# Optimization experiments

Measured on AMD Instinct MI355X. Metric: run time of the kernel, lower is better.

The kernel has to match this reference:

```python
import jax, jax.numpy as jnp
import numpy as np

B, S, D, I, E = 2, 2048, 1024, 2048, 8
AUX_COEF, Z_COEF = 0.01, 0.001


def setup_inputs() -> dict:
    key = jax.random.key(0)
    ks = jax.random.split(key, 5)
    sd = np.float32(1.0 / np.sqrt(D))
    si = np.float32(1.0 / np.sqrt(I))
    return {
        "hidden_states": jax.random.normal(ks[0], (B, S, D), jnp.float32),
        "gate_w": jax.random.normal(ks[1], (D, E), jnp.float32) * sd,
        "w_gate": jax.random.normal(ks[2], (E, D, I), jnp.float32) * sd,
        "w_up": jax.random.normal(ks[3], (E, D, I), jnp.float32) * sd,
        "w_down": jax.random.normal(ks[4], (E, I, D), jnp.float32) * si,
        "pressure_bias": jnp.zeros((E,), jnp.float32),
        "temperature_field": jnp.ones((E,), jnp.float32),
    }


def reference(hidden_states, gate_w, w_gate, w_up, w_down, pressure_bias, temperature_field):
    b, s, d = hidden_states.shape
    e = gate_w.shape[1]
    x = hidden_states.reshape(-1, d)  # [T, D]

    # Router with P/T geometry: logits' = (logits + P) / clamp(T)
    logits = x @ gate_w + pressure_bias
    temp = jnp.clip(temperature_field, 0.1, 10.0)
    logits = logits / temp
    probs = jax.nn.softmax(logits, axis=-1)  # [T, E]
    routing_weights = jnp.max(probs, axis=-1)  # [T]
    selected = jnp.argmax(probs, axis=-1)      # [T] int

    # Load balancing + z-loss
    onehot = jax.nn.one_hot(selected, e, dtype=probs.dtype)
    f_i = onehot.mean(axis=0)          # fraction of tokens per expert
    P_i = probs.mean(axis=0)           # mean routing prob per expert
    load_balance = e * jnp.sum(f_i * P_i)
    z_loss = jnp.mean(jax.nn.logsumexp(logits, axis=-1) ** 2)
    aux_loss = AUX_COEF * load_balance + Z_COEF * z_loss

    # Top-1 dispatch/combine: row-wise SwiGLU FFN, mask non-selected rows.
    out = jnp.zeros_like(x)
    for ei in range(e):  # small fixed expert count
        y = (jax.nn.silu(x @ w_gate[ei]) * (x @ w_up[ei])) @ w_down[ei]
        out = out + jnp.where((selected == ei)[:, None], y * routing_weights[:, None], 0.0)

    return out.reshape(b, s, d), aux_loss
```

## Files before the change

kernel.cpp:

```cpp
#include <hip/hip_runtime.h>
#include <stdint.h>
#include <stddef.h>

#define T_TOK 4096
#define D_DIM 1024
#define I_DIM 2048
#define E_EXP 8

#define MAXT64  (T_TOK / 64 + E_EXP)
#define MAXT128 (T_TOK / 128 + E_EXP)
#define CAP (T_TOK + E_EXP * 128)

#define BT 64
#define NK1 (D_DIM / BT)
#define NC1 (I_DIM / BT)
#define G1_BLOCKS (MAXT64 * NC1)
#define BM2 128
#define BN2 64
#define BK2 64
#define NK2 (I_DIM / BK2)
#define NC2 (D_DIM / BN2)

typedef __attribute__((ext_vector_type(4))) float f32x4;
typedef __attribute__((ext_vector_type(4))) short s16x4;
typedef __attribute__((ext_vector_type(8))) short s16x8;
typedef __attribute__((ext_vector_type(2))) unsigned int u32x2;

__device__ __forceinline__ unsigned short f2bf(float f) {
    union { float f; unsigned u; } v; v.f = f;
    unsigned u = v.u;
    return (unsigned short)((u + 0x7fffu + ((u >> 16) & 1u)) >> 16);
}

__device__ __forceinline__ void gll16(const void* g, void* l) {
    __builtin_amdgcn_global_load_lds(
        (const __attribute__((address_space(1))) void*)g,
        (__attribute__((address_space(3))) void*)l, 16, 0, 0);
}

__global__ void k_init(int* idxl, int* counts, int* fill, float* sumP, float* lse2) {
    int tid = blockIdx.x * blockDim.x + threadIdx.x;
    for (int i = tid; i < CAP; i += blockDim.x * gridDim.x) idxl[i] = -1;
    if (blockIdx.x == 0 && threadIdx.x < E_EXP) {
        counts[threadIdx.x] = 0;
        fill[threadIdx.x] = 0;
        sumP[threadIdx.x] = 0.f;
    }
    if (blockIdx.x == 0 && threadIdx.x == 0) lse2[0] = 0.f;
}

__device__ void router_block(
    const float* __restrict__ x, const float* __restrict__ gw,
    const float* __restrict__ pb, const float* __restrict__ tf,
    unsigned short* __restrict__ xb, int* __restrict__ selected,
    float* __restrict__ rw, int* __restrict__ counts,
    float* __restrict__ sumP, float* __restrict__ lse2)
{
    int gwave = (blockIdx.x * 256 + threadIdx.x) >> 6;
    int lane = threadIdx.x & 63;

    float aP[E_EXP];
    int aC[E_EXP];
    float aZ = 0.f;
#pragma unroll
    for (int e = 0; e < E_EXP; e++) { aP[e] = 0.f; aC[e] = 0; }

    float tcl[E_EXP], pbv[E_EXP];
#pragma unroll
    for (int e = 0; e < E_EXP; e++) {
        tcl[e] = fminf(fmaxf(tf[e], 0.1f), 10.f);
        pbv[e] = pb[e];
    }

    for (int ti = 0; ti < 16; ++ti) {
        int t = gwave * 16 + ti;
        const float* xr = x + (size_t)t * D_DIM;
        float s[E_EXP];
#pragma unroll
        for (int e = 0; e < E_EXP; e++) s[e] = 0.f;

#pragma unroll
        for (int j = 0; j < 4; j++) {
            int d0 = j * 256 + lane * 4;
            f32x4 xv = *(const f32x4*)(xr + d0);
            s16x4 xs;
#pragma unroll
            for (int i = 0; i < 4; i++) xs[i] = (short)f2bf(xv[i]);
            *(s16x4*)(xb + (size_t)t * D_DIM + d0) = xs;
#pragma unroll
            for (int i = 0; i < 4; i++) {
                const float* gr = gw + (size_t)(d0 + i) * E_EXP;
                f32x4 g0 = *(const f32x4*)(gr);
                f32x4 g1 = *(const f32x4*)(gr + 4);
                float xi = xv[i];
                s[0] += xi * g0[0]; s[1] += xi * g0[1];
                s[2] += xi * g0[2]; s[3] += xi * g0[3];
                s[4] += xi * g1[0]; s[5] += xi * g1[1];
                s[6] += xi * g1[2]; s[7] += xi * g1[3];
            }
        }
#pragma unroll
        for (int m = 1; m < 64; m <<= 1) {
#pragma unroll
            for (int e = 0; e < E_EXP; e++) s[e] += __shfl_xor(s[e], m, 64);
        }
        float lg[E_EXP];
        float mx = -3.4e38f;
#pragma unroll
        for (int e = 0; e < E_EXP; e++) {
            lg[e] = (s[e] + pbv[e]) / tcl[e];
            mx = fmaxf(mx, lg[e]);
        }
        float p[E_EXP];
        float den = 0.f;
#pragma unroll
        for (int e = 0; e < E_EXP; e++) { p[e] = expf(lg[e] - mx); den += p[e]; }
        int sel = 0;
        float best = lg[0];
#pragma unroll
        for (int e = 1; e < E_EXP; e++) if (lg[e] > best) { best = lg[e]; sel = e; }
        float inv = 1.f / den;
        if (lane == 0) {
            selected[t] = sel;
            rw[t] = p[sel] * inv;
#pragma unroll
            for (int e = 0; e < E_EXP; e++) aP[e] += p[e] * inv;
            aC[sel] += 1;
            float lse = mx + logf(den);
            aZ += lse * lse;
        }
    }
    if (lane == 0) {
#pragma unroll
        for (int e = 0; e < E_EXP; e++) {
            atomicAdd(&sumP[e], aP[e]);
            if (aC[e]) atomicAdd(&counts[e], aC[e]);
        }
        atomicAdd(lse2, aZ);
    }
}

__device__ void conv_tile(const float* __restrict__ src, unsigned short* __restrict__ dst,
                          int R, int C, int rt, int ct, unsigned short* tb)
{
    int r0 = rt * 128, c0 = ct * 128;
    int tid = threadIdx.x;
    int rr = tid >> 5;
    int cc = (tid & 31) * 4;

#pragma unroll
    for (int p = 0; p < 16; ++p) {
        int r = p * 8 + rr;
        f32x4 v = *(const f32x4*)(src + (size_t)(r0 + r) * C + c0 + cc);
        s16x4 w;
#pragma unroll
        for (int i = 0; i < 4; ++i) w[i] = (short)f2bf(v[i]);
        *(s16x4*)(tb + r * 130 + cc) = w;
    }
    __syncthreads();

    int rb = (tid & 15) * 4;
    int cp = (tid >> 4) * 2;
#pragma unroll
    for (int p = 0; p < 8; ++p) {
        int rh = (p & 1) * 64;
        int c = (p >> 1) * 32 + cp;
        int rbase = rh + rb;
        unsigned int a0 = *(const unsigned int*)(tb + (rbase + 0) * 130 + c);
        unsigned int a1 = *(const unsigned int*)(tb + (rbase + 1) * 130 + c);
        unsigned int a2 = *(const unsigned int*)(tb + (rbase + 2) * 130 + c);
        unsigned int a3 = *(const unsigned int*)(tb + (rbase + 3) * 130 + c);
        u32x2 lo, hi;
        lo[0] = (a0 & 0xffffu) | (a1 << 16);
        lo[1] = (a2 & 0xffffu) | (a3 << 16);
        hi[0] = (a0 >> 16) | (a1 & 0xffff0000u);
        hi[1] = (a2 >> 16) | (a3 & 0xffff0000u);
        *(u32x2*)(dst + (size_t)(c0 + c) * R + r0 + rbase) = lo;
        *(u32x2*)(dst + (size_t)(c0 + c + 1) * R + r0 + rbase) = hi;
    }
}

__global__ __launch_bounds__(256) void k_fused1(
    const float* __restrict__ x, const float* __restrict__ gw,
    const float* __restrict__ pb, const float* __restrict__ tf,
    unsigned short* __restrict__ xb, int* __restrict__ selected,
    float* __restrict__ rw, int* __restrict__ counts,
    float* __restrict__ sumP, float* __restrict__ lse2,
    const float* __restrict__ wg, const float* __restrict__ wu,
    unsigned short* __restrict__ wgT, unsigned short* __restrict__ wuT)
{
    __shared__ unsigned short tb[128 * 130];
    int bid = blockIdx.x;
    if (bid < 64) {
        router_block(x, gw, pb, tf, xb, selected, rw, counts, sumP, lse2);
        return;
    }
    int b = bid - 64;
    if (b < 1024) {
        int e = b >> 7, t = b & 127;
        conv_tile(wg + (size_t)e * D_DIM * I_DIM, wgT + (size_t)e * D_DIM * I_DIM,
                  D_DIM, I_DIM, t >> 4, t & 15, tb);
    } else {
        b -= 1024;
        int e = b >> 7, t = b & 127;
        conv_tile(wu + (size_t)e * D_DIM * I_DIM, wuT + (size_t)e * D_DIM * I_DIM,
                  D_DIM, I_DIM, t >> 4, t & 15, tb);
    }
}

__global__ void k_setup(const int* counts, int* segst,
                        int* t128e, int* t128b, int* t64e, int* t64b) {
    if (threadIdx.x == 0 && blockIdx.x == 0) {
        int off = 0, a = 0, b = 0;
        for (int e = 0; e < E_EXP; e++) {
            segst[e] = off;
            int n = counts[e];
            int n128 = (n + 127) >> 7;
            int n64 = (n + 63) >> 6;
            for (int i = 0; i < n128; i++) { t128e[a] = e; t128b[a] = off + i * 128; a++; }
            for (int i = 0; i < n64; i++)  { t64e[b] = e;  t64b[b] = off + i * 64;  b++; }
            off += n128 * 128;
        }
        for (; a < MAXT128; ++a) { t128e[a] = -1; t128b[a] = 0; }
        for (; b < MAXT64; ++b)  { t64e[b] = -1;  t64b[b] = 0; }
    }
}

__global__ void k_scatter(const int* selected, const int* segst, int* fill, int* idxl) {
    int t = blockIdx.x * 256 + threadIdx.x;
    if (t < T_TOK) {
        int e = selected[t];
        int p = atomicAdd(&fill[e], 1);
        idxl[segst[e] + p] = t;
    }
}

__global__ __launch_bounds__(256) void k_fused2(
    const unsigned short* __restrict__ xb,
    const unsigned short* __restrict__ wgT,
    const int* __restrict__ idxl,
    const int* __restrict__ t64e, const int* __restrict__ t64b,
    unsigned short* __restrict__ H,
    const float* __restrict__ wd, unsigned short* __restrict__ wdT)
{
    __shared__ union {
        struct {
            unsigned short As[2][BT * BT];
            unsigned short Bg[2][BT * BT];
            unsigned short Bu[2][BT * BT];
        } g;
        unsigned short tb[128 * 130];
    } sm;

    int bid = blockIdx.x;
    int gid;
    if (bid < 2048) {
        if (bid & 1) {
            int b = bid >> 1;
            int e = b >> 7, t = b & 127;
            conv_tile(wd + (size_t)e * I_DIM * D_DIM, wdT + (size_t)e * I_DIM * D_DIM,
                      I_DIM, D_DIM, t >> 3, t & 7, sm.tb);
            return;
        }
        gid = bid >> 1;
    } else {
        gid = 1024 + (bid - 2048);
    }

    int rt = gid >> 5;
    int ct = gid & 31;
    int e = t64e[rt];
    if (e < 0) return;
    int base = t64b[rt];

    int tid = threadIdx.x;
    int l = tid & 63;
    int w = tid >> 6;
    int rsub = l >> 3;
    int csw = ((l & 7) ^ rsub) * 8;

    int tk0 = idxl[base + w * 16 + rsub];     tk0 = tk0 < 0 ? 0 : tk0;
    int tk1 = idxl[base + w * 16 + 8 + rsub]; tk1 = tk1 < 0 ? 0 : tk1;
    const unsigned short* gA0 = xb + (size_t)tk0 * D_DIM + csw;
    const unsigned short* gA1 = xb + (size_t)tk1 * D_DIM + csw;
    const size_t WOFF = (size_t)E_EXP * I_DIM * D_DIM;
    const unsigned short* gB0 = wgT + ((size_t)e * I_DIM + ct * 64 + w * 16 + rsub) * D_DIM + csw;
    const unsigned short* gB1 = gB0 + (size_t)8 * D_DIM;
    int aoff = w * 1024;

#define STAGE1(buf, ko) do { \
        gll16(gA0 + (ko), &sm.g.As[buf][aoff]); \
        gll16(gA1 + (ko), &sm.g.As[buf][aoff + 512]); \
        gll16(gB0 + (ko), &sm.g.Bg[buf][aoff]); \
        gll16(gB1 + (ko), &sm.g.Bg[buf][aoff + 512]); \
        gll16(gB0 + WOFF + (ko), &sm.g.Bu[buf][aoff]); \
        gll16(gB1 + WOFF + (ko), &sm.g.Bu[buf][aoff + 512]); \
    } while (0)

    int wm = (w >> 1) * 32;
    int wn = (w & 1) * 32;
    int lr = l & 15;
    int lxor = l & 7;

    f32x4 zero4 = {0.f, 0.f, 0.f, 0.f};
    f32x4 accG[2][2], accU[2][2];
#pragma unroll
    for (int i = 0; i < 2; i++)
#pragma unroll
        for (int j = 0; j < 2; j++) { accG[i][j] = zero4; accU[i][j] = zero4; }

    STAGE1(0, 0);
    __syncthreads();

    for (int kt = 0; kt < NK1; ++kt) {
        if (kt + 1 < NK1) STAGE1((kt + 1) & 1, (kt + 1) * BT);
        int b = kt & 1;
#pragma unroll
        for (int ks = 0; ks < 2; ++ks) {
            int kx = ((ks * 4 + (l >> 4)) ^ lxor) * 8;
            s16x8 af[2], bg[2], bu[2];
#pragma unroll
            for (int mi = 0; mi < 2; mi++)
                af[mi] = *(const s16x8*)(&sm.g.As[b][(wm + mi * 16 + lr) * 64 + kx]);
#pragma unroll
            for (int ni = 0; ni < 2; ni++) {
                bg[ni] = *(const s16x8*)(&sm.g.Bg[b][(wn + ni * 16 + lr) * 64 + kx]);
                bu[ni] = *(const s16x8*)(&sm.g.Bu[b][(wn + ni * 16 + lr) * 64 + kx]);
            }
#pragma unroll
            for (int mi = 0; mi < 2; mi++)
#pragma unroll
                for (int ni = 0; ni < 2; ni++) {
                    accG[mi][ni] = __builtin_amdgcn_mfma_f32_16x16x32_bf16(af[mi], bg[ni], accG[mi][ni], 0, 0, 0);
                    accU[mi][ni] = __builtin_amdgcn_mfma_f32_16x16x32_bf16(af[mi], bu[ni], accU[mi][ni], 0, 0, 0);
                }
        }
        __syncthreads();
    }
#undef STAGE1

#pragma unroll
    for (int mi = 0; mi < 2; mi++) {
#pragma unroll
        for (int r = 0; r < 4; r++) {
            int row = wm + mi * 16 + (l >> 4) * 4 + r;
            unsigned short* hr = H + (size_t)(base + row) * I_DIM + ct * 64 + wn + lr;
#pragma unroll
            for (int ni = 0; ni < 2; ni++) {
                float g = accG[mi][ni][r];
                float u = accU[mi][ni][r];
                float h = (g / (1.f + expf(-g))) * u;
                hr[ni * 16] = f2bf(h);
            }
        }
    }
}

__global__ __launch_bounds__(256) void k_gemm2(
    const unsigned short* __restrict__ H,
    const unsigned short* __restrict__ wdT,
    const int* __restrict__ idxl, const float* __restrict__ rw,
    const int* __restrict__ t128e, const int* __restrict__ t128b,
    float* __restrict__ out)
{
    __shared__ unsigned short As2[2][BM2 * BK2];
    __shared__ unsigned short Bs2[2][BN2 * BK2];
    __shared__ int s_tok[BM2];
    __shared__ float s_rw[BM2];

    int bid = blockIdx.x;
    int rt = bid >> 4;
    int ct = bid & 15;
    int e = t128e[rt];
    if (e < 0) return;
    int base = t128b[rt];

    int tid = threadIdx.x;
    int lane = tid & 63;
    int wid = tid >> 6;

    if (tid < BM2) {
        int tk = idxl[base + tid];
        s_tok[tid] = tk;
        s_rw[tid] = (tk >= 0) ? rw[tk] : 0.f;
    }

    int rsub = lane >> 3;
    int csw = ((lane & 7) ^ rsub) * 8;
    int ar = wid * 32 + rsub;
    const unsigned short* gA = H + (size_t)(base + ar) * I_DIM + csw;
    int br = wid * 16 + rsub;
    const unsigned short* gB = wdT + ((size_t)e * D_DIM + (size_t)ct * BN2 + br) * I_DIM + csw;

    int aoff = wid * 32 * BK2;
    int boff = wid * 16 * BK2;

#define STAGE2(buf, ko) do { \
        gll16(gA + (ko),                      &As2[buf][aoff]); \
        gll16(gA + (size_t)8  * I_DIM + (ko), &As2[buf][aoff + 8 * BK2]); \
        gll16(gA + (size_t)16 * I_DIM + (ko), &As2[buf][aoff + 16 * BK2]); \
        gll16(gA + (size_t)24 * I_DIM + (ko), &As2[buf][aoff + 24 * BK2]); \
        gll16(gB + (ko),                      &Bs2[buf][boff]); \
        gll16(gB + (size_t)8 * I_DIM + (ko),  &Bs2[buf][boff + 8 * BK2]); \
    } while (0)

    int wm = (wid >> 1) * 64;
    int wn = (wid & 1) * 32;
    int lr = lane & 15;
    int lxor = lane & 7;

    f32x4 zero4 = {0.f, 0.f, 0.f, 0.f};
    f32x4 acc[4][2];
#pragma unroll
    for (int i = 0; i < 4; i++)
#pragma unroll
        for (int j = 0; j < 2; j++) acc[i][j] = zero4;

    STAGE2(0, 0);
    __syncthreads();

    for (int kt = 0; kt < NK2; ++kt) {
        if (kt + 1 < NK2) STAGE2((kt + 1) & 1, (kt + 1) * BK2);
        int b = kt & 1;
#pragma unroll
        for (int ks = 0; ks < 2; ++ks) {
            int kx = ((ks * 4 + (lane >> 4)) ^ lxor) * 8;
            s16x8 af[4], bf[2];
#pragma unroll
            for (int mi = 0; mi < 4; mi++)
                af[mi] = *(const s16x8*)&As2[b][(wm + mi * 16 + lr) * BK2 + kx];
#pragma unroll
            for (int ni = 0; ni < 2; ni++)
                bf[ni] = *(const s16x8*)&Bs2[b][(wn + ni * 16 + lr) * BK2 + kx];
#pragma unroll
            for (int mi = 0; mi < 4; mi++)
#pragma unroll
                for (int ni = 0; ni < 2; ni++)
                    acc[mi][ni] = __builtin_amdgcn_mfma_f32_16x16x32_bf16(af[mi], bf[ni], acc[mi][ni], 0, 0, 0);
        }
        __syncthreads();
    }
#undef STAGE2

#pragma unroll
    for (int mi = 0; mi < 4; mi++) {
#pragma unroll
        for (int r = 0; r < 4; r++) {
            int row = wm + mi * 16 + (lane >> 4) * 4 + r;
            int tk = s_tok[row];
            if (tk >= 0) {
                float scale = s_rw[row];
                float* orow = out + (size_t)tk * D_DIM + (size_t)ct * BN2 + wn + lr;
#pragma unroll
                for (int ni = 0; ni < 2; ni++)
                    orow[ni * 16] = acc[mi][ni][r] * scale;
            }
        }
    }
}

__global__ void k_aux(const int* counts, const float* sumP, const float* lse2, float* out) {
    if (threadIdx.x == 0 && blockIdx.x == 0) {
        float lb = 0.f;
        for (int e = 0; e < E_EXP; e++) {
            float f = (float)counts[e] / (float)T_TOK;
            float P = sumP[e] / (float)T_TOK;
            lb += f * P;
        }
        float aux = 0.01f * ((float)E_EXP * lb) + 0.001f * (lse2[0] / (float)T_TOK);
        out[(size_t)T_TOK * D_DIM] = aux;
    }
}

extern "C" void kernel_launch(void* const* d_in, const int* in_sizes, int n_in,
                              void* d_out, int out_size, void* d_ws, size_t ws_size,
                              hipStream_t stream)
{
    const float* x      = (const float*)d_in[0];
    const float* gw     = (const float*)d_in[1];
    const float* w_gate = (const float*)d_in[2];
    const float* w_up   = (const float*)d_in[3];
    const float* w_down = (const float*)d_in[4];
    const float* pb     = (const float*)d_in[5];
    const float* tf     = (const float*)d_in[6];
    float* out = (float*)d_out;

    char* ws = (char*)d_ws;
    int*   selected = (int*)ws;
    float* rwp      = (float*)(selected + T_TOK);
    int*   idxl     = (int*)(rwp + T_TOK);
    int*   counts   = idxl + CAP;
    int*   fill     = counts + E_EXP;
    int*   segst    = fill + E_EXP;
    int*   t128e    = segst + E_EXP;
    int*   t128b    = t128e + MAXT128;
    int*   t64e     = t128b + MAXT128;
    int*   t64b     = t64e + MAXT64;
    float* sumP     = (float*)(t64b + MAXT64);
    float* lse2     = sumP + E_EXP;

    const size_t XB_OFF  = 65536;
    const size_t H_OFF   = XB_OFF + (size_t)T_TOK * D_DIM * 2;
    const size_t WGT_OFF = H_OFF + (size_t)CAP * I_DIM * 2;
    const size_t WUT_OFF = WGT_OFF + (size_t)E_EXP * I_DIM * D_DIM * 2;
    const size_t WDT_OFF = WUT_OFF + (size_t)E_EXP * I_DIM * D_DIM * 2;

    unsigned short* xb  = (unsigned short*)(ws + XB_OFF);
    unsigned short* H   = (unsigned short*)(ws + H_OFF);
    unsigned short* wgT = (unsigned short*)(ws + WGT_OFF);
    unsigned short* wuT = (unsigned short*)(ws + WUT_OFF);
    unsigned short* wdT = (unsigned short*)(ws + WDT_OFF);

    k_init<<<dim3(8), dim3(256), 0, stream>>>(idxl, counts, fill, sumP, lse2);
    k_fused1<<<dim3(64 + 2048), dim3(256), 0, stream>>>(
        x, gw, pb, tf, xb, selected, rwp, counts, sumP, lse2,
        w_gate, w_up, wgT, wuT);
    k_setup<<<dim3(1), dim3(64), 0, stream>>>(counts, segst, t128e, t128b, t64e, t64b);
    k_scatter<<<dim3(16), dim3(256), 0, stream>>>(selected, segst, fill, idxl);
    k_fused2<<<dim3(G1_BLOCKS + 1024), dim3(256), 0, stream>>>(
        xb, wgT, idxl, t64e, t64b, H, w_down, wdT);
    k_gemm2<<<dim3(MAXT128 * NC2), dim3(256), 0, stream>>>(H, wdT, idxl, rwp, t128e, t128b, out);
    k_aux<<<dim3(1), dim3(64), 0, stream>>>(counts, sumP, lse2, out);
}
```

Baseline: 225.5 us.

## Enlarge gate/up GEMM tile to 128x128 and rebalance fused w_down conversion

Grows the first expert GEMM from 64x64 to 128x128 output tiles, with a 4x4 MFMA block per wave for both gate and up. This gives more data reuse per shared-memory load and halves the weight re-reads. It drops the double-buffered shared-memory pipeline in favour of a single buffer with a sync after each load. It also reassigns the interleaved w_down transpose/convert blocks so that all 1024 conversion tiles still run, and changes the conv_tile write pattern. The costs are more registers (64 accumulators per thread), lower occupancy and exposed load latency now that prefetch is gone.

```diff
diff --git a/kernel.cpp b/kernel.cpp
--- a/kernel.cpp
+++ b/kernel.cpp
@@ -11,10 +11,9 @@
 #define MAXT128 (T_TOK / 128 + E_EXP)
 #define CAP (T_TOK + E_EXP * 128)
 
-#define BT 64
-#define NK1 (D_DIM / BT)
-#define NC1 (I_DIM / BT)
-#define G1_BLOCKS (MAXT64 * NC1)
+#define NK1 (D_DIM / 64)
+#define NC1 (I_DIM / 128)
+#define G1_BLOCKS (MAXT128 * NC1)
 #define BM2 128
 #define BN2 64
 #define BK2 64
@@ -159,24 +158,22 @@
     }
     __syncthreads();
 
-    int rb = (tid & 15) * 4;
-    int cp = (tid >> 4) * 2;
+    int rb = (tid & 31) * 4;
+    int cb = (tid >> 5) * 2;
 #pragma unroll
     for (int p = 0; p < 8; ++p) {
-        int rh = (p & 1) * 64;
-        int c = (p >> 1) * 32 + cp;
-        int rbase = rh + rb;
-        unsigned int a0 = *(const unsigned int*)(tb + (rbase + 0) * 130 + c);
-        unsigned int a1 = *(const unsigned int*)(tb + (rbase + 1) * 130 + c);
-        unsigned int a2 = *(const unsigned int*)(tb + (rbase + 2) * 130 + c);
-        unsigned int a3 = *(const unsigned int*)(tb + (rbase + 3) * 130 + c);
+        int c = p * 16 + cb;
+        unsigned int a0 = *(const unsigned int*)(tb + (rb + 0) * 130 + c);
+        unsigned int a1 = *(const unsigned int*)(tb + (rb + 1) * 130 + c);
+        unsigned int a2 = *(const unsigned int*)(tb + (rb + 2) * 130 + c);
+        unsigned int a3 = *(const unsigned int*)(tb + (rb + 3) * 130 + c);
         u32x2 lo, hi;
         lo[0] = (a0 & 0xffffu) | (a1 << 16);
         lo[1] = (a2 & 0xffffu) | (a3 << 16);
         hi[0] = (a0 >> 16) | (a1 & 0xffff0000u);
         hi[1] = (a2 >> 16) | (a3 & 0xffff0000u);
-        *(u32x2*)(dst + (size_t)(c0 + c) * R + r0 + rbase) = lo;
-        *(u32x2*)(dst + (size_t)(c0 + c + 1) * R + r0 + rbase) = hi;
+        *(u32x2*)(dst + (size_t)(c0 + c) * R + r0 + rb) = lo;
+        *(u32x2*)(dst + (size_t)(c0 + c + 1) * R + r0 + rb) = hi;
     }
 }
 
@@ -239,23 +236,23 @@
     const unsigned short* __restrict__ xb,
     const unsigned short* __restrict__ wgT,
     const int* __restrict__ idxl,
-    const int* __restrict__ t64e, const int* __restrict__ t64b,
+    const int* __restrict__ t128e, const int* __restrict__ t128b,
     unsigned short* __restrict__ H,
     const float* __restrict__ wd, unsigned short* __restrict__ wdT)
 {
     __shared__ union {
         struct {
-            unsigned short As[2][BT * BT];
-            unsigned short Bg[2][BT * BT];
-            unsigned short Bu[2][BT * BT];
+            unsigned short As[128 * 64];
+            unsigned short Bg[128 * 64];
+            unsigned short Bu[128 * 64];
         } g;
         unsigned short tb[128 * 130];
     } sm;
 
     int bid = blockIdx.x;
     int gid;
-    if (bid < 2048) {
-        if (bid & 1) {
+    if (bid < 2 * G1_BLOCKS) {
+        if ((bid & 1) == 0) {
             int b = bid >> 1;
             int e = b >> 7, t = b & 127;
             conv_tile(wd + (size_t)e * I_DIM * D_DIM, wdT + (size_t)e * I_DIM * D_DIM,
@@ -264,89 +261,93 @@
         }
         gid = bid >> 1;
     } else {
-        gid = 1024 + (bid - 2048);
-    }
-
-    int rt = gid >> 5;
-    int ct = gid & 31;
-    int e = t64e[rt];
+        int b = 640 + (bid - 2 * G1_BLOCKS);
+        int e = b >> 7, t = b & 127;
+        conv_tile(wd + (size_t)e * I_DIM * D_DIM, wdT + (size_t)e * I_DIM * D_DIM,
+                  I_DIM, D_DIM, t >> 3, t & 7, sm.tb);
+        return;
+    }
+
+    int rt = gid >> 4;
+    int ct = gid & 15;
+    int e = t128e[rt];
     if (e < 0) return;
-    int base = t64b[rt];
+    int base = t128b[rt];
 
     int tid = threadIdx.x;
     int l = tid & 63;
     int w = tid >> 6;
-    int rsub = l >> 3;
-    int csw = ((l & 7) ^ rsub) * 8;
-
-    int tk0 = idxl[base + w * 16 + rsub];     tk0 = tk0 < 0 ? 0 : tk0;
-    int tk1 = idxl[base + w * 16 + 8 + rsub]; tk1 = tk1 < 0 ? 0 : tk1;
-    const unsigned short* gA0 = xb + (size_t)tk0 * D_DIM + csw;
-    const unsigned short* gA1 = xb + (size_t)tk1 * D_DIM + csw;
+    int ls3 = l >> 3;
+    int csw = ((l & 7) ^ ls3) * 8;
+
+    const unsigned short* gA[4];
+    const unsigned short* gB[4];
+#pragma unroll
+    for (int i = 0; i < 4; ++i) {
+        int r = w * 32 + ls3 + i * 8;
+        int tk = idxl[base + r]; tk = tk < 0 ? 0 : tk;
+        gA[i] = xb + (size_t)tk * D_DIM + csw;
+        gB[i] = wgT + ((size_t)e * I_DIM + ct * 128 + r) * D_DIM + csw;
+    }
     const size_t WOFF = (size_t)E_EXP * I_DIM * D_DIM;
-    const unsigned short* gB0 = wgT + ((size_t)e * I_DIM + ct * 64 + w * 16 + rsub) * D_DIM + csw;
-    const unsigned short* gB1 = gB0 + (size_t)8 * D_DIM;
-    int aoff = w * 1024;
-
-#define STAGE1(buf, ko) do { \
-        gll16(gA0 + (ko), &sm.g.As[buf][aoff]); \
-        gll16(gA1 + (ko), &sm.g.As[buf][aoff + 512]); \
-        gll16(gB0 + (ko), &sm.g.Bg[buf][aoff]); \
-        gll16(gB1 + (ko), &sm.g.Bg[buf][aoff + 512]); \
-        gll16(gB0 + WOFF + (ko), &sm.g.Bu[buf][aoff]); \
-        gll16(gB1 + WOFF + (ko), &sm.g.Bu[buf][aoff + 512]); \
+    int aoff = w * 2048 + l * 8;
+
+#define STG1(ko) do { \
+        _Pragma("unroll") \
+        for (int i = 0; i < 4; ++i) { \
+            gll16(gA[i] + (ko), sm.g.As + aoff + i * 512); \
+            gll16(gB[i] + (ko), sm.g.Bg + aoff + i * 512); \
+            gll16(gB[i] + WOFF + (ko), sm.g.Bu + aoff + i * 512); \
+        } \
     } while (0)
 
-    int wm = (w >> 1) * 32;
-    int wn = (w & 1) * 32;
+    int wm = (w >> 1) * 64;
+    int wn = (w & 1) * 64;
     int lr = l & 15;
-    int lxor = l & 7;
+    int lx = lr & 7;
 
     f32x4 zero4 = {0.f, 0.f, 0.f, 0.f};
-    f32x4 accG[2][2], accU[2][2];
-#pragma unroll
-    for (int i = 0; i < 2; i++)
-#pragma unroll
-        for (int j = 0; j < 2; j++) { accG[i][j] = zero4; accU[i][j] = zero4; }
-
-    STAGE1(0, 0);
-    __syncthreads();
+    f32x4 accG[4][4], accU[4][4];
+#pragma unroll
+    for (int i = 0; i < 4; i++)
+#pragma unroll
+        for (int j = 0; j < 4; j++) { accG[i][j] = zero4; accU[i][j] = zero4; }
 
     for (int kt = 0; kt < NK1; ++kt) {
-        if (kt + 1 < NK1) STAGE1((kt + 1) & 1, (kt + 1) * BT);
-        int b = kt & 1;
+        STG1(kt * 64);
+        __syncthreads();
 #pragma unroll
         for (int ks = 0; ks < 2; ++ks) {
-            int kx = ((ks * 4 + (l >> 4)) ^ lxor) * 8;
-            s16x8 af[2], bg[2], bu[2];
-#pragma unroll
-            for (int mi = 0; mi < 2; mi++)
-                af[mi] = *(const s16x8*)(&sm.g.As[b][(wm + mi * 16 + lr) * 64 + kx]);
-#pragma unroll
-            for (int ni = 0; ni < 2; ni++) {
-                bg[ni] = *(const s16x8*)(&sm.g.Bg[b][(wn + ni * 16 + lr) * 64 + kx]);
-                bu[ni] = *(const s16x8*)(&sm.g.Bu[b][(wn + ni * 16 + lr) * 64 + kx]);
+            int kx = ((ks * 4 + (l >> 4)) ^ lx) * 8;
+            s16x8 af[4], bg[4], bu[4];
+#pragma unroll
+            for (int mi = 0; mi < 4; mi++)
+                af[mi] = *(const s16x8*)(sm.g.As + (wm + mi * 16 + lr) * 64 + kx);
+#pragma unroll
+            for (int ni = 0; ni < 4; ni++) {
+                bg[ni] = *(const s16x8*)(sm.g.Bg + (wn + ni * 16 + lr) * 64 + kx);
+                bu[ni] = *(const s16x8*)(sm.g.Bu + (wn + ni * 16 + lr) * 64 + kx);
             }
 #pragma unroll
-            for (int mi = 0; mi < 2; mi++)
-#pragma unroll
-                for (int ni = 0; ni < 2; ni++) {
+            for (int mi = 0; mi < 4; mi++)
+#pragma unroll
+                for (int ni = 0; ni < 4; ni++) {
                     accG[mi][ni] = __builtin_amdgcn_mfma_f32_16x16x32_bf16(af[mi], bg[ni], accG[mi][ni], 0, 0, 0);
                     accU[mi][ni] = __builtin_amdgcn_mfma_f32_16x16x32_bf16(af[mi], bu[ni], accU[mi][ni], 0, 0, 0);
                 }
         }
         __syncthreads();
     }
-#undef STAGE1
-
-#pragma unroll
-    for (int mi = 0; mi < 2; mi++) {
+#undef STG1
+
+#pragma unroll
+    for (int mi = 0; mi < 4; mi++) {
 #pragma unroll
         for (int r = 0; r < 4; r++) {
             int row = wm + mi * 16 + (l >> 4) * 4 + r;
-            unsigned short* hr = H + (size_t)(base + row) * I_DIM + ct * 64 + wn + lr;
-#pragma unroll
-            for (int ni = 0; ni < 2; ni++) {
+            unsigned short* hr = H + (size_t)(base + row) * I_DIM + ct * 128 + wn + lr;
+#pragma unroll
+            for (int ni = 0; ni < 4; ni++) {
                 float g = accG[mi][ni][r];
                 float u = accU[mi][ni][r];
                 float h = (g / (1.f + expf(-g))) * u;
@@ -517,8 +518,8 @@
         w_gate, w_up, wgT, wuT);
     k_setup<<<dim3(1), dim3(64), 0, stream>>>(counts, segst, t128e, t128b, t64e, t64b);
     k_scatter<<<dim3(16), dim3(256), 0, stream>>>(selected, segst, fill, idxl);
-    k_fused2<<<dim3(G1_BLOCKS + 1024), dim3(256), 0, stream>>>(
-        xb, wgT, idxl, t64e, t64b, H, w_down, wdT);
+    k_fused2<<<dim3(2 * G1_BLOCKS + (1024 - G1_BLOCKS)), dim3(256), 0, stream>>>(
+        xb, wgT, idxl, t128e, t128b, H, w_down, wdT);
     k_gemm2<<<dim3(MAXT128 * NC2), dim3(256), 0, stream>>>(H, wdT, idxl, rwp, t128e, t128b, out);
     k_aux<<<dim3(1), dim3(64), 0, stream>>>(counts, sumP, lse2, out);
 }
```

Result: slower. 307.5 us (+36.4%).
